# Optimization experiments

Measured on AMD Instinct MI355X. Metric: run time of the kernel, lower is better.

The kernel has to match this reference:

```python
import jax, jax.numpy as jnp
import numpy as np

N = 65536      # tokens
D = 512        # input_dim
H = 8          # num_heads
HD = 64        # head_dim
FF = 2048      # hidden_dim
EPS = 1e-5


def _layer_norm(x, g, b):
    mu = jnp.mean(x, axis=-1, keepdims=True)
    var = jnp.mean(jnp.square(x - mu), axis=-1, keepdims=True)
    return (x - mu) * jax.lax.rsqrt(var + EPS) * g + b


def setup_inputs() -> dict:
    key = jax.random.key(0)
    ks = jax.random.split(key, 12)
    s_d = 1.0 / np.sqrt(D)
    s_f = 1.0 / np.sqrt(FF)
    return {
        "x":   jax.random.normal(ks[0], (N, D), jnp.float32),
        # Linear weights stored [in, out] (transpose of torch's [out, in])
        "Wq":  jax.random.uniform(ks[1], (D, D), jnp.float32, -s_d, s_d),
        "bq":  jnp.zeros((D,), jnp.float32),
        "Wk":  jax.random.uniform(ks[2], (D, D), jnp.float32, -s_d, s_d),
        "bk":  jnp.zeros((D,), jnp.float32),
        "Wv":  jax.random.uniform(ks[3], (D, D), jnp.float32, -s_d, s_d),
        "bv":  jnp.zeros((D,), jnp.float32),
        "ln1_g": jnp.ones((D,), jnp.float32),
        "ln1_b": jnp.zeros((D,), jnp.float32),
        "W1":  jax.random.uniform(ks[4], (D, FF), jnp.float32, -s_d, s_d),
        "b1":  jnp.zeros((FF,), jnp.float32),
        "W2":  jax.random.uniform(ks[5], (FF, D), jnp.float32, -s_f, s_f),
        "b2":  jnp.zeros((D,), jnp.float32),
        "ln2_g": jnp.ones((D,), jnp.float32),
        "ln2_b": jnp.zeros((D,), jnp.float32),
    }


def reference(x, Wq, bq, Wk, bk, Wv, bv, ln1_g, ln1_b, W1, b1, W2, b2, ln2_g, ln2_b):
    n = x.shape[0]
    # --- multi-head attention (per-token head mixing, as in source) ---
    q = (x @ Wq + bq).reshape(n, H, HD)
    k = (x @ Wk + bk).reshape(n, H, HD)
    v = (x @ Wv + bv).reshape(n, H, HD)
    # score[n] = q[n] @ k[n]^T : [H, H] per token
    score = jnp.einsum("nhd,ngd->nhg", q, k) / jnp.sqrt(jnp.float32(HD))
    attn = jax.nn.softmax(score, axis=-1)
    ctx = jnp.einsum("nhg,ngd->nhd", attn, v).reshape(n, D)
    y = _layer_norm(x + ctx, ln1_g, ln1_b)
    # --- feed forward with residual + layer norm ---
    h = jax.nn.relu(y @ W1 + b1)
    z = h @ W2 + b2 + y
    return _layer_norm(z, ln2_g, ln2_b)
```

## Files before the change

kernel.cpp:

```cpp
#include <hip/hip_runtime.h>
#include <cstdint>


typedef __attribute__((ext_vector_type(8))) short bf16x8;
typedef __attribute__((ext_vector_type(4))) float f32x4;
typedef __attribute__((ext_vector_type(8))) unsigned short u16x8;

__device__ __forceinline__ float bf2f(unsigned short u) {
  union { unsigned int i; float f; } v; v.i = ((unsigned int)u) << 16; return v.f;
}
__device__ __forceinline__ unsigned short f2bf(float f) {
  union { float f; unsigned int i; } v; v.f = f;
  unsigned int r = v.i + 0x7FFFu + ((v.i >> 16) & 1u);
  return (unsigned short)(r >> 16);
}

#define GLD16(g, l)                                                         \
  __builtin_amdgcn_global_load_lds(                                         \
      (const __attribute__((address_space(1))) void*)(g),                   \
      (__attribute__((address_space(3))) void*)(l), 16, 0, 0)

__global__ __launch_bounds__(256) void cast_f32_bf16(
    const float* __restrict__ in, ushort* __restrict__ out) {
  const size_t i = (size_t)blockIdx.x * 256 + threadIdx.x;
  const float4* p = (const float4*)in + i * 2;
  float4 a = p[0], b = p[1];
  u16x8 r;
  r[0] = f2bf(a.x); r[1] = f2bf(a.y); r[2] = f2bf(a.z); r[3] = f2bf(a.w);
  r[4] = f2bf(b.x); r[5] = f2bf(b.y); r[6] = f2bf(b.z); r[7] = f2bf(b.w);
  ((u16x8*)out)[i] = r;
}

__global__ __launch_bounds__(256) void transpose_cast(
    const float* __restrict__ W, ushort* __restrict__ Wt,
    int K, int Nn, int rowoff, int ldt) {
  __shared__ float tile[32][33];
  const int tx = threadIdx.x & 31, ty = threadIdx.x >> 5;
  const int nb = blockIdx.x * 32, kb = blockIdx.y * 32;
#pragma unroll
  for (int s = 0; s < 4; ++s)
    tile[ty + 8 * s][tx] = W[(size_t)(kb + ty + 8 * s) * Nn + nb + tx];
  __syncthreads();
#pragma unroll
  for (int s = 0; s < 4; ++s)
    Wt[(size_t)(rowoff + nb + ty + 8 * s) * ldt + kb + tx] =
        f2bf(tile[tx][ty + 8 * s]);
}

template <int EPI>
__global__ __launch_bounds__(512, 2) void gemm_bt(
    const ushort* __restrict__ A, const ushort* __restrict__ Bt,
    int N, int K, void* __restrict__ Cout,
    const float* __restrict__ bias0, const float* __restrict__ bias1,
    const float* __restrict__ bias2, const ushort* __restrict__ resid) {
  constexpr int BK = 32;
  __shared__ __align__(16) ushort lds[4 * 16384];
  const int tid = threadIdx.x;
  const int wid = tid >> 6, lane = tid & 63;
  const int wm = wid >> 2, wn = wid & 3;

  const int gx = gridDim.x;
  const int nwg = gx * gridDim.y;
  const int orig = blockIdx.y * gx + blockIdx.x;
  const int q = nwg >> 3, r = nwg & 7;
  const int xcd = orig & 7, loc = orig >> 3;
  const int swz = (xcd < r) ? (xcd * (q + 1) + loc)
                            : (r * (q + 1) + (xcd - r) * q + loc);
  const size_t m0 = (size_t)(swz / gx) * 256;
  const size_t n0 = (size_t)(swz % gx) * 256;
  const int NT = K / BK;

  const int sgcol = (((tid & 3) - ((tid >> 3) & 3)) & 3) << 3;
  const ushort* a0 = A + (m0 + (tid >> 2)) * (size_t)K + sgcol;
  const ushort* b0 = Bt + (n0 + (tid >> 2)) * (size_t)K + sgcol;
  const size_t rowK = 128 * (size_t)K;
  ushort* ldst = &lds[tid * 8];

#define STAGE_A(t)                                                          \
  {                                                                         \
    ushort* d = ldst + ((t) & 3) * 16384;                                   \
    const ushort* g = a0 + (size_t)(t) * BK;                                \
    GLD16(g, d);                                                            \
    GLD16(g + rowK, d + 4096);                                              \
  }
#define STAGE_B(t)                                                          \
  {                                                                         \
    ushort* d = ldst + ((t) & 3) * 16384 + 8192;                            \
    const ushort* g = b0 + (size_t)(t) * BK;                                \
    GLD16(g, d);                                                            \
    GLD16(g + rowK, d + 4096);                                              \
  }

  const int cswz = ((((lane >> 4) + ((lane >> 1) & 3)) & 3) << 3);
  const int arow = wm * 128 + (lane & 15);
  const int brow = wn * 64 + (lane & 15);

  f32x4 acc[8][4] = {};

  STAGE_A(0); STAGE_B(0);
  STAGE_A(1); STAGE_B(1);
  STAGE_A(2); STAGE_B(2);

  for (int t = 0; t < NT; ++t) {
    if (t < NT - 2) {
      asm volatile("s_waitcnt vmcnt(8)" ::: "memory");
    } else if (t == NT - 2) {
      asm volatile("s_waitcnt vmcnt(4)" ::: "memory");
    } else {
      asm volatile("s_waitcnt vmcnt(0)" ::: "memory");
    }
    __builtin_amdgcn_s_barrier();

    const ushort* lA = &lds[(t & 3) * 16384];
    const ushort* lB = lA + 8192;

    bf16x8 af[4], bfr[4];
#pragma unroll
    for (int mi = 0; mi < 4; ++mi)
      af[mi] = *(const bf16x8*)&lA[(arow + mi * 16) * 32 + cswz];
#pragma unroll
    for (int ni = 0; ni < 4; ++ni)
      bfr[ni] = *(const bf16x8*)&lB[(brow + ni * 16) * 32 + cswz];
    if (t + 3 < NT) STAGE_A(t + 3);
    __builtin_amdgcn_s_setprio(1);
#pragma unroll
    for (int mi = 0; mi < 4; ++mi)
#pragma unroll
      for (int ni = 0; ni < 4; ++ni)
        acc[mi][ni] = __builtin_amdgcn_mfma_f32_16x16x32_bf16(
            af[mi], bfr[ni], acc[mi][ni], 0, 0, 0);
    __builtin_amdgcn_s_setprio(0);
    __builtin_amdgcn_s_barrier();

    bf16x8 ag[4];
#pragma unroll
    for (int mi = 0; mi < 4; ++mi)
      ag[mi] = *(const bf16x8*)&lA[(arow + (mi + 4) * 16) * 32 + cswz];
    if (t + 3 < NT) STAGE_B(t + 3);
    __builtin_amdgcn_s_setprio(1);
#pragma unroll
    for (int mi = 0; mi < 4; ++mi)
#pragma unroll
      for (int ni = 0; ni < 4; ++ni)
        acc[mi + 4][ni] = __builtin_amdgcn_mfma_f32_16x16x32_bf16(
            ag[mi], bfr[ni], acc[mi + 4][ni], 0, 0, 0);
    __builtin_amdgcn_s_setprio(0);
  }
#undef STAGE_A
#undef STAGE_B

  const int lm = lane & 15, lq = lane >> 4;
  size_t col[4];
  float bv[4];
#pragma unroll
  for (int ni = 0; ni < 4; ++ni) {
    col[ni] = n0 + wn * 64 + ni * 16 + lm;
    if (EPI == 0) {
      const float* bp = (n0 < 512) ? bias0 : ((n0 < 1024) ? bias1 : bias2);
      bv[ni] = bp[col[ni] & 511];
    } else {
      bv[ni] = bias0[col[ni]];
    }
  }
#pragma unroll
  for (int mi = 0; mi < 8; ++mi) {
#pragma unroll
    for (int j = 0; j < 4; ++j) {
      const size_t row = m0 + wm * 128 + mi * 16 + lq * 4 + j;
#pragma unroll
      for (int ni = 0; ni < 4; ++ni) {
        float v = acc[mi][ni][j] + bv[ni];
        if (EPI == 0) {
          ((ushort*)Cout)[row * N + col[ni]] = f2bf(v);
        } else if (EPI == 1) {
          ((ushort*)Cout)[row * N + col[ni]] = f2bf(fmaxf(v, 0.f));
        } else {
          v += bf2f(resid[row * N + col[ni]]);
          ((float*)Cout)[row * N + col[ni]] = v;
        }
      }
    }
  }
}

__global__ __launch_bounds__(256) void attn_ln1(
    const ushort* __restrict__ qkv, const float* __restrict__ x,
    const float* __restrict__ g1, const float* __restrict__ b1,
    ushort* __restrict__ y) {
  const int lane = threadIdx.x & 63;
  const size_t t = (size_t)blockIdx.x * 4 + (threadIdx.x >> 6);
  const ushort* base = qkv + t * 1536;
  float qd[8], kd[8], vd[8];
#pragma unroll
  for (int h = 0; h < 8; ++h) {
    qd[h] = bf2f(base[h * 64 + lane]);
    kd[h] = bf2f(base[512 + h * 64 + lane]);
    vd[h] = bf2f(base[1024 + h * 64 + lane]);
  }

  const bool lb0 = lane & 1, lb1 = lane & 2, lb2 = lane & 4;
  const bool lb3 = lane & 8, lb4 = lane & 16, lb5 = lane & 32;

  float c1[32];
#pragma unroll
  for (int f = 0; f < 32; ++f) {
    const int i0 = 2 * f, i1 = 2 * f + 1;
    const float a0 = qd[i0 >> 3] * kd[i0 & 7];
    const float a1 = qd[i1 >> 3] * kd[i1 & 7];
    const float keep = lb0 ? a1 : a0;
    const float send = lb0 ? a0 : a1;
    c1[f] = keep + __shfl_xor(send, 1, 64);
  }
  float c2[16];
#pragma unroll
  for (int f = 0; f < 16; ++f) {
    const float keep = lb1 ? c1[2 * f + 1] : c1[2 * f];
    const float send = lb1 ? c1[2 * f] : c1[2 * f + 1];
    c2[f] = keep + __shfl_xor(send, 2, 64);
  }
  float c3[8];
#pragma unroll
  for (int f = 0; f < 8; ++f) {
    const float keep = lb2 ? c2[2 * f + 1] : c2[2 * f];
    const float send = lb2 ? c2[2 * f] : c2[2 * f + 1];
    c3[f] = keep + __shfl_xor(send, 4, 64);
  }
  float c4[4];
#pragma unroll
  for (int f = 0; f < 4; ++f) {
    const float keep = lb3 ? c3[2 * f + 1] : c3[2 * f];
    const float send = lb3 ? c3[2 * f] : c3[2 * f + 1];
    c4[f] = keep + __shfl_xor(send, 8, 64);
  }
  float c5[2];
#pragma unroll
  for (int f = 0; f < 2; ++f) {
    const float keep = lb4 ? c4[2 * f + 1] : c4[2 * f];
    const float send = lb4 ? c4[2 * f] : c4[2 * f + 1];
    c5[f] = keep + __shfl_xor(send, 16, 64);
  }
  const float keep = lb5 ? c5[1] : c5[0];
  const float send = lb5 ? c5[0] : c5[1];
  const float s = keep + __shfl_xor(send, 32, 64);

  float mx = s;
  mx = fmaxf(mx, __shfl_xor(mx, 1, 64));
  mx = fmaxf(mx, __shfl_xor(mx, 2, 64));
  mx = fmaxf(mx, __shfl_xor(mx, 4, 64));
  const float e = __expf((s - mx) * 0.125f);
  float sum = e;
  sum += __shfl_xor(sum, 1, 64);
  sum += __shfl_xor(sum, 2, 64);
  sum += __shfl_xor(sum, 4, 64);
  const float a = e * __builtin_amdgcn_rcpf(sum);

  const int ai = __float_as_int(a);
  float r[8];
#pragma unroll
  for (int h = 0; h < 8; ++h) {
    float c = 0.f;
#pragma unroll
    for (int g = 0; g < 8; ++g) {
      const float w = __int_as_float(__builtin_amdgcn_readlane(ai, h * 8 + g));
      c = fmaf(w, vd[g], c);
    }
    r[h] = x[t * 512 + h * 64 + lane] + c;
  }

  float sm = 0.f, sq = 0.f;
#pragma unroll
  for (int h = 0; h < 8; ++h) { sm += r[h]; sq += r[h] * r[h]; }
#pragma unroll
  for (int m = 1; m < 64; m <<= 1) {
    sm += __shfl_xor(sm, m, 64);
    sq += __shfl_xor(sq, m, 64);
  }
  const float mu = sm * (1.f / 512.f);
  const float var = sq * (1.f / 512.f) - mu * mu;
  const float rs = rsqrtf(var + 1e-5f);
#pragma unroll
  for (int h = 0; h < 8; ++h) {
    const int d = h * 64 + lane;
    y[t * 512 + d] = f2bf((r[h] - mu) * rs * g1[d] + b1[d]);
  }
}

__global__ __launch_bounds__(256) void ln_out(
    const float* __restrict__ z, const float* __restrict__ g2,
    const float* __restrict__ b2, float* __restrict__ out) {
  const int lane = threadIdx.x & 63;
  const size_t t = (size_t)blockIdx.x * 4 + (threadIdx.x >> 6);
  const float4* zp = (const float4*)(z + t * 512);
  const float4 r0 = zp[lane], r1 = zp[lane + 64];
  float sm = r0.x + r0.y + r0.z + r0.w + r1.x + r1.y + r1.z + r1.w;
  float sq = r0.x * r0.x + r0.y * r0.y + r0.z * r0.z + r0.w * r0.w +
             r1.x * r1.x + r1.y * r1.y + r1.z * r1.z + r1.w * r1.w;
#pragma unroll
  for (int m = 1; m < 64; m <<= 1) {
    sm += __shfl_xor(sm, m, 64);
    sq += __shfl_xor(sq, m, 64);
  }
  const float mu = sm * (1.f / 512.f);
  const float rs = rsqrtf(sq * (1.f / 512.f) - mu * mu + 1e-5f);
  const float4* g4 = (const float4*)g2;
  const float4* b4 = (const float4*)b2;
  float4* o4 = (float4*)(out + t * 512);
  const float4 ga = g4[lane], gb = g4[lane + 64];
  const float4 ba = b4[lane], bb = b4[lane + 64];
  float4 oa, ob;
  oa.x = (r0.x - mu) * rs * ga.x + ba.x;
  oa.y = (r0.y - mu) * rs * ga.y + ba.y;
  oa.z = (r0.z - mu) * rs * ga.z + ba.z;
  oa.w = (r0.w - mu) * rs * ga.w + ba.w;
  ob.x = (r1.x - mu) * rs * gb.x + bb.x;
  ob.y = (r1.y - mu) * rs * gb.y + bb.y;
  ob.z = (r1.z - mu) * rs * gb.z + bb.z;
  ob.w = (r1.w - mu) * rs * gb.w + bb.w;
  o4[lane] = oa;
  o4[lane + 64] = ob;
}

extern "C" void kernel_launch(void* const* d_in, const int* in_sizes, int n_in,
                              void* d_out, int out_size, void* d_ws,
                              size_t ws_size, hipStream_t stream) {
  const float* x    = (const float*)d_in[0];
  const float* Wq   = (const float*)d_in[1];
  const float* bq   = (const float*)d_in[2];
  const float* Wk   = (const float*)d_in[3];
  const float* bk   = (const float*)d_in[4];
  const float* Wv   = (const float*)d_in[5];
  const float* bv   = (const float*)d_in[6];
  const float* ln1g = (const float*)d_in[7];
  const float* ln1b = (const float*)d_in[8];
  const float* W1   = (const float*)d_in[9];
  const float* b1   = (const float*)d_in[10];
  const float* W2   = (const float*)d_in[11];
  const float* b2   = (const float*)d_in[12];
  const float* ln2g = (const float*)d_in[13];
  const float* ln2b = (const float*)d_in[14];
  float* out = (float*)d_out;

  const int Ntok = in_sizes[0] / 512;

  char* ws = (char*)d_ws;
  ushort* Wqkvt = (ushort*)ws;
  ushort* W1t   = Wqkvt + (size_t)1536 * 512;
  ushort* W2t   = W1t + (size_t)2048 * 512;
  const size_t woff = ((size_t)1536 * 512 + (size_t)2048 * 512 +
                       (size_t)512 * 2048) * 2;

  size_t avail = (ws_size > woff) ? (ws_size - woff) : 0;
  long long Cll = (long long)(avail / 9216);
  Cll = (Cll / 256) * 256;
  if (Cll > 32768) Cll = 32768;
  if (Cll > Ntok) Cll = Ntok;
  if (Cll < 256) Cll = 256;
  const int C = (int)Cll;

  char* cb = ws + woff;
  ushort* xb  = (ushort*)cb;
  ushort* y   = xb + (size_t)C * 512;
  ushort* qkv = y + (size_t)C * 512;
  ushort* hb  = qkv + (size_t)C * 1536;
  float*  z   = (float*)qkv;

  transpose_cast<<<dim3(16, 16), dim3(256), 0, stream>>>(Wq, Wqkvt, 512, 512, 0, 512);
  transpose_cast<<<dim3(16, 16), dim3(256), 0, stream>>>(Wk, Wqkvt, 512, 512, 512, 512);
  transpose_cast<<<dim3(16, 16), dim3(256), 0, stream>>>(Wv, Wqkvt, 512, 512, 1024, 512);
  transpose_cast<<<dim3(64, 16), dim3(256), 0, stream>>>(W1, W1t, 512, 2048, 0, 512);
  transpose_cast<<<dim3(16, 64), dim3(256), 0, stream>>>(W2, W2t, 2048, 512, 0, 2048);

  for (int t0 = 0; t0 < Ntok; t0 += C) {
    const int Cc = (Ntok - t0 < C) ? (Ntok - t0) : C;
    const float* xc = x + (size_t)t0 * 512;

    cast_f32_bf16<<<dim3((Cc * 512) / 2048), dim3(256), 0, stream>>>(xc, xb);

    gemm_bt<0><<<dim3(1536 / 256, Cc / 256), dim3(512), 0, stream>>>(
        xb, Wqkvt, 1536, 512, qkv, bq, bk, bv, nullptr);

    attn_ln1<<<dim3(Cc / 4), dim3(256), 0, stream>>>(qkv, xc, ln1g, ln1b, y);

    gemm_bt<1><<<dim3(2048 / 256, Cc / 256), dim3(512), 0, stream>>>(
        y, W1t, 2048, 512, hb, b1, nullptr, nullptr, nullptr);

    gemm_bt<2><<<dim3(512 / 256, Cc / 256), dim3(512), 0, stream>>>(
        hb, W2t, 512, 2048, z, b2, nullptr, nullptr, y);

    ln_out<<<dim3(Cc / 4), dim3(256), 0, stream>>>(
        z, ln2g, ln2b, out + (size_t)t0 * 512);
  }
}
```

Baseline: 666.8 us.

## Make GEMM persistent with cross-tile prefetch pipeline over 256 workgroups

Converts the tiled GEMM into a persistent kernel launched with 256 workgroups, each looping over output tiles strided by 256 and treating all k-steps of all its tiles as one continuous pipeline. Loads for the next tile are issued during the previous tile's tail, so the prologue/epilogue bubbles and per-block launch cost are removed, and the epilogue runs inline before the accumulators are zeroed. It drops the XCD-aware tile swizzle, hardcodes ntLog for only K=512 or 2048, and stores the epilogue while the next prefetches are in flight, which may hurt L2 locality and register pressure.

```diff
diff --git a/kernel.cpp b/kernel.cpp
--- a/kernel.cpp
+++ b/kernel.cpp
@@ -50,7 +50,7 @@
 template <int EPI>
 __global__ __launch_bounds__(512, 2) void gemm_bt(
     const ushort* __restrict__ A, const ushort* __restrict__ Bt,
-    int N, int K, void* __restrict__ Cout,
+    int M, int N, int K, void* __restrict__ Cout,
     const float* __restrict__ bias0, const float* __restrict__ bias1,
     const float* __restrict__ bias2, const ushort* __restrict__ resid) {
   constexpr int BK = 32;
@@ -59,34 +59,42 @@
   const int wid = tid >> 6, lane = tid & 63;
   const int wm = wid >> 2, wn = wid & 3;
 
-  const int gx = gridDim.x;
-  const int nwg = gx * gridDim.y;
-  const int orig = blockIdx.y * gx + blockIdx.x;
-  const int q = nwg >> 3, r = nwg & 7;
-  const int xcd = orig & 7, loc = orig >> 3;
-  const int swz = (xcd < r) ? (xcd * (q + 1) + loc)
-                            : (r * (q + 1) + (xcd - r) * q + loc);
-  const size_t m0 = (size_t)(swz / gx) * 256;
-  const size_t n0 = (size_t)(swz % gx) * 256;
+  const int NX = N >> 8;
+  const int tiles = (M >> 8) * NX;
+  const int b = blockIdx.x;
+  const int nOut = (tiles - b + 255) >> 8;
+  if (nOut <= 0) return;
   const int NT = K / BK;
+  const int ntLog = (NT == 16) ? 4 : 6;
+  const int Ttot = nOut * NT;
 
   const int sgcol = (((tid & 3) - ((tid >> 3) & 3)) & 3) << 3;
-  const ushort* a0 = A + (m0 + (tid >> 2)) * (size_t)K + sgcol;
-  const ushort* b0 = Bt + (n0 + (tid >> 2)) * (size_t)K + sgcol;
+  const int thrRow = tid >> 2;
   const size_t rowK = 128 * (size_t)K;
   ushort* ldst = &lds[tid * 8];
 
-#define STAGE_A(t)                                                          \
+#define TILE_COORDS(tau, sm0, sn0, sk0)                                     \
+  const int ot_ = (tau) >> ntLog;                                           \
+  const int T_ = b + (ot_ << 8);                                            \
+  const size_t sm0 = (size_t)(T_ / NX) << 8;                                \
+  const size_t sn0 = (size_t)(T_ % NX) << 8;                                \
+  const size_t sk0 = (size_t)((tau) & (NT - 1)) * BK;
+
+#define STAGE_A(tau)                                                        \
   {                                                                         \
-    ushort* d = ldst + ((t) & 3) * 16384;                                   \
-    const ushort* g = a0 + (size_t)(t) * BK;                                \
+    TILE_COORDS(tau, sm0, sn0, sk0)                                         \
+    (void)sn0;                                                              \
+    const ushort* g = A + (sm0 + thrRow) * (size_t)K + sgcol + sk0;         \
+    ushort* d = ldst + ((tau) & 3) * 16384;                                 \
     GLD16(g, d);                                                            \
     GLD16(g + rowK, d + 4096);                                              \
   }
-#define STAGE_B(t)                                                          \
+#define STAGE_B(tau)                                                        \
   {                                                                         \
-    ushort* d = ldst + ((t) & 3) * 16384 + 8192;                            \
-    const ushort* g = b0 + (size_t)(t) * BK;                                \
+    TILE_COORDS(tau, sm0, sn0, sk0)                                         \
+    (void)sm0;                                                              \
+    const ushort* g = Bt + (sn0 + thrRow) * (size_t)K + sgcol + sk0;        \
+    ushort* d = ldst + ((tau) & 3) * 16384 + 8192;                          \
     GLD16(g, d);                                                            \
     GLD16(g + rowK, d + 4096);                                              \
   }
@@ -94,6 +102,7 @@
   const int cswz = ((((lane >> 4) + ((lane >> 1) & 3)) & 3) << 3);
   const int arow = wm * 128 + (lane & 15);
   const int brow = wn * 64 + (lane & 15);
+  const int lm = lane & 15, lq = lane >> 4;
 
   f32x4 acc[8][4] = {};
 
@@ -101,17 +110,17 @@
   STAGE_A(1); STAGE_B(1);
   STAGE_A(2); STAGE_B(2);
 
-  for (int t = 0; t < NT; ++t) {
-    if (t < NT - 2) {
+  for (int tau = 0; tau < Ttot; ++tau) {
+    if (tau < Ttot - 2) {
       asm volatile("s_waitcnt vmcnt(8)" ::: "memory");
-    } else if (t == NT - 2) {
+    } else if (tau == Ttot - 2) {
       asm volatile("s_waitcnt vmcnt(4)" ::: "memory");
     } else {
       asm volatile("s_waitcnt vmcnt(0)" ::: "memory");
     }
     __builtin_amdgcn_s_barrier();
 
-    const ushort* lA = &lds[(t & 3) * 16384];
+    const ushort* lA = &lds[(tau & 3) * 16384];
     const ushort* lB = lA + 8192;
 
     bf16x8 af[4], bfr[4];
@@ -121,7 +130,7 @@
 #pragma unroll
     for (int ni = 0; ni < 4; ++ni)
       bfr[ni] = *(const bf16x8*)&lB[(brow + ni * 16) * 32 + cswz];
-    if (t + 3 < NT) STAGE_A(t + 3);
+    if (tau + 3 < Ttot) STAGE_A(tau + 3);
     __builtin_amdgcn_s_setprio(1);
 #pragma unroll
     for (int mi = 0; mi < 4; ++mi)
@@ -136,7 +145,7 @@
 #pragma unroll
     for (int mi = 0; mi < 4; ++mi)
       ag[mi] = *(const bf16x8*)&lA[(arow + (mi + 4) * 16) * 32 + cswz];
-    if (t + 3 < NT) STAGE_B(t + 3);
+    if (tau + 3 < Ttot) STAGE_B(tau + 3);
     __builtin_amdgcn_s_setprio(1);
 #pragma unroll
     for (int mi = 0; mi < 4; ++mi)
@@ -145,42 +154,52 @@
         acc[mi + 4][ni] = __builtin_amdgcn_mfma_f32_16x16x32_bf16(
             ag[mi], bfr[ni], acc[mi + 4][ni], 0, 0, 0);
     __builtin_amdgcn_s_setprio(0);
+
+    if ((tau & (NT - 1)) == NT - 1) {
+      TILE_COORDS(tau, m0, n0, k0)
+      (void)k0;
+      size_t col[4];
+      float bv[4];
+#pragma unroll
+      for (int ni = 0; ni < 4; ++ni) {
+        col[ni] = n0 + wn * 64 + ni * 16 + lm;
+        if (EPI == 0) {
+          const float* bp = (n0 < 512) ? bias0 : ((n0 < 1024) ? bias1 : bias2);
+          bv[ni] = bp[col[ni] & 511];
+        } else {
+          bv[ni] = bias0[col[ni]];
+        }
+      }
+#pragma unroll
+      for (int mi = 0; mi < 8; ++mi) {
+#pragma unroll
+        for (int j = 0; j < 4; ++j) {
+          const size_t row = m0 + wm * 128 + mi * 16 + lq * 4 + j;
+#pragma unroll
+          for (int ni = 0; ni < 4; ++ni) {
+            float v = acc[mi][ni][j] + bv[ni];
+            if (EPI == 0) {
+              ((ushort*)Cout)[row * N + col[ni]] = f2bf(v);
+            } else if (EPI == 1) {
+              ((ushort*)Cout)[row * N + col[ni]] = f2bf(fmaxf(v, 0.f));
+            } else {
+              v += bf2f(resid[row * N + col[ni]]);
+              ((float*)Cout)[row * N + col[ni]] = v;
+            }
+          }
+        }
+      }
+#pragma unroll
+      for (int mi = 0; mi < 8; ++mi)
+#pragma unroll
+        for (int ni = 0; ni < 4; ++ni)
+#pragma unroll
+          for (int j = 0; j < 4; ++j) acc[mi][ni][j] = 0.f;
+    }
   }
 #undef STAGE_A
 #undef STAGE_B
-
-  const int lm = lane & 15, lq = lane >> 4;
-  size_t col[4];
-  float bv[4];
-#pragma unroll
-  for (int ni = 0; ni < 4; ++ni) {
-    col[ni] = n0 + wn * 64 + ni * 16 + lm;
-    if (EPI == 0) {
-      const float* bp = (n0 < 512) ? bias0 : ((n0 < 1024) ? bias1 : bias2);
-      bv[ni] = bp[col[ni] & 511];
-    } else {
-      bv[ni] = bias0[col[ni]];
-    }
-  }
-#pragma unroll
-  for (int mi = 0; mi < 8; ++mi) {
-#pragma unroll
-    for (int j = 0; j < 4; ++j) {
-      const size_t row = m0 + wm * 128 + mi * 16 + lq * 4 + j;
-#pragma unroll
-      for (int ni = 0; ni < 4; ++ni) {
-        float v = acc[mi][ni][j] + bv[ni];
-        if (EPI == 0) {
-          ((ushort*)Cout)[row * N + col[ni]] = f2bf(v);
-        } else if (EPI == 1) {
-          ((ushort*)Cout)[row * N + col[ni]] = f2bf(fmaxf(v, 0.f));
-        } else {
-          v += bf2f(resid[row * N + col[ni]]);
-          ((float*)Cout)[row * N + col[ni]] = v;
-        }
-      }
-    }
-  }
+#undef TILE_COORDS
 }
 
 __global__ __launch_bounds__(256) void attn_ln1(
@@ -376,16 +395,16 @@
 
     cast_f32_bf16<<<dim3((Cc * 512) / 2048), dim3(256), 0, stream>>>(xc, xb);
 
-    gemm_bt<0><<<dim3(1536 / 256, Cc / 256), dim3(512), 0, stream>>>(
-        xb, Wqkvt, 1536, 512, qkv, bq, bk, bv, nullptr);
+    gemm_bt<0><<<dim3(256), dim3(512), 0, stream>>>(
+        xb, Wqkvt, Cc, 1536, 512, qkv, bq, bk, bv, nullptr);
 
     attn_ln1<<<dim3(Cc / 4), dim3(256), 0, stream>>>(qkv, xc, ln1g, ln1b, y);
 
-    gemm_bt<1><<<dim3(2048 / 256, Cc / 256), dim3(512), 0, stream>>>(
-        y, W1t, 2048, 512, hb, b1, nullptr, nullptr, nullptr);
-
-    gemm_bt<2><<<dim3(512 / 256, Cc / 256), dim3(512), 0, stream>>>(
-        hb, W2t, 512, 2048, z, b2, nullptr, nullptr, y);
+    gemm_bt<1><<<dim3(256), dim3(512), 0, stream>>>(
+        y, W1t, Cc, 2048, 512, hb, b1, nullptr, nullptr, nullptr);
+
+    gemm_bt<2><<<dim3(256), dim3(512), 0, stream>>>(
+        hb, W2t, Cc, 512, 2048, z, b2, nullptr, nullptr, y);
 
     ln_out<<<dim3(Cc / 4), dim3(256), 0, stream>>>(
         z, ln2g, ln2b, out + (size_t)t0 * 512);
```

Result: slower. 690.3 us (+3.5%).

## Split GEMM k-step into four barrier phases and store FFN output as bf16

Applied to the files above, without the earlier changes.

The GEMM main loop now runs as four phases per k-step. Each phase loads two A fragments, issues one quarter of the next tile's global-to-LDS loads, and runs eight MFMAs between barriers, so loads are spread more evenly against compute. The second FFN GEMM now writes its residual-added output as bf16 instead of fp32, and ln_out reads bf16, which halves that intermediate traffic. attn_ln1 now reads the bf16 copy of x for the residual instead of fp32, trading precision for less bandwidth. The extra barriers per k-step add synchronisation cost.

```diff
diff --git a/kernel.cpp b/kernel.cpp
--- a/kernel.cpp
+++ b/kernel.cpp
@@ -62,10 +62,10 @@
   const int gx = gridDim.x;
   const int nwg = gx * gridDim.y;
   const int orig = blockIdx.y * gx + blockIdx.x;
-  const int q = nwg >> 3, r = nwg & 7;
+  const int q8 = nwg >> 3, r8 = nwg & 7;
   const int xcd = orig & 7, loc = orig >> 3;
-  const int swz = (xcd < r) ? (xcd * (q + 1) + loc)
-                            : (r * (q + 1) + (xcd - r) * q + loc);
+  const int swz = (xcd < r8) ? (xcd * (q8 + 1) + loc)
+                             : (r8 * (q8 + 1) + (xcd - r8) * q8 + loc);
   const size_t m0 = (size_t)(swz / gx) * 256;
   const size_t n0 = (size_t)(swz % gx) * 256;
   const int NT = K / BK;
@@ -76,19 +76,12 @@
   const size_t rowK = 128 * (size_t)K;
   ushort* ldst = &lds[tid * 8];
 
-#define STAGE_A(t)                                                          \
+#define STAGE_SLOT(t, sl)                                                   \
   {                                                                         \
-    ushort* d = ldst + ((t) & 3) * 16384;                                   \
-    const ushort* g = a0 + (size_t)(t) * BK;                                \
+    ushort* d = ldst + ((t) & 3) * 16384 + (sl) * 4096;                     \
+    const ushort* g = (((sl) < 2) ? a0 : b0) + (size_t)(t) * BK +           \
+                      (((sl) & 1) ? rowK : 0);                              \
     GLD16(g, d);                                                            \
-    GLD16(g + rowK, d + 4096);                                              \
-  }
-#define STAGE_B(t)                                                          \
-  {                                                                         \
-    ushort* d = ldst + ((t) & 3) * 16384 + 8192;                            \
-    const ushort* g = b0 + (size_t)(t) * BK;                                \
-    GLD16(g, d);                                                            \
-    GLD16(g + rowK, d + 4096);                                              \
   }
 
   const int cswz = ((((lane >> 4) + ((lane >> 1) & 3)) & 3) << 3);
@@ -97,9 +90,30 @@
 
   f32x4 acc[8][4] = {};
 
-  STAGE_A(0); STAGE_B(0);
-  STAGE_A(1); STAGE_B(1);
-  STAGE_A(2); STAGE_B(2);
+#pragma unroll
+  for (int pt = 0; pt < 3; ++pt) {
+    STAGE_SLOT(pt, 0); STAGE_SLOT(pt, 1);
+    STAGE_SLOT(pt, 2); STAGE_SLOT(pt, 3);
+  }
+
+#define PHASE(pi)                                                           \
+  {                                                                         \
+    bf16x8 y0 = *(const bf16x8*)&lA[(arow + (2 * (pi)) * 16) * 32 + cswz];  \
+    bf16x8 y1 = *(const bf16x8*)&lA[(arow + (2 * (pi) + 1) * 16) * 32 + cswz]; \
+    if (pf) STAGE_SLOT(t3, pi);                                             \
+    __builtin_amdgcn_s_barrier();                                           \
+    __builtin_amdgcn_s_setprio(1);                                          \
+    _Pragma("unroll")                                                       \
+    for (int ni = 0; ni < 4; ++ni)                                          \
+      acc[2 * (pi)][ni] = __builtin_amdgcn_mfma_f32_16x16x32_bf16(          \
+          y0, bfr[ni], acc[2 * (pi)][ni], 0, 0, 0);                         \
+    _Pragma("unroll")                                                       \
+    for (int ni = 0; ni < 4; ++ni)                                          \
+      acc[2 * (pi) + 1][ni] = __builtin_amdgcn_mfma_f32_16x16x32_bf16(      \
+          y1, bfr[ni], acc[2 * (pi) + 1][ni], 0, 0, 0);                     \
+    __builtin_amdgcn_s_setprio(0);                                          \
+    __builtin_amdgcn_s_barrier();                                           \
+  }
 
   for (int t = 0; t < NT; ++t) {
     if (t < NT - 2) {
@@ -113,41 +127,21 @@
 
     const ushort* lA = &lds[(t & 3) * 16384];
     const ushort* lB = lA + 8192;
-
-    bf16x8 af[4], bfr[4];
-#pragma unroll
-    for (int mi = 0; mi < 4; ++mi)
-      af[mi] = *(const bf16x8*)&lA[(arow + mi * 16) * 32 + cswz];
+    const bool pf = (t + 3 < NT);
+    const int t3 = t + 3;
+
+    bf16x8 bfr[4];
 #pragma unroll
     for (int ni = 0; ni < 4; ++ni)
       bfr[ni] = *(const bf16x8*)&lB[(brow + ni * 16) * 32 + cswz];
-    if (t + 3 < NT) STAGE_A(t + 3);
-    __builtin_amdgcn_s_setprio(1);
-#pragma unroll
-    for (int mi = 0; mi < 4; ++mi)
-#pragma unroll
-      for (int ni = 0; ni < 4; ++ni)
-        acc[mi][ni] = __builtin_amdgcn_mfma_f32_16x16x32_bf16(
-            af[mi], bfr[ni], acc[mi][ni], 0, 0, 0);
-    __builtin_amdgcn_s_setprio(0);
-    __builtin_amdgcn_s_barrier();
-
-    bf16x8 ag[4];
-#pragma unroll
-    for (int mi = 0; mi < 4; ++mi)
-      ag[mi] = *(const bf16x8*)&lA[(arow + (mi + 4) * 16) * 32 + cswz];
-    if (t + 3 < NT) STAGE_B(t + 3);
-    __builtin_amdgcn_s_setprio(1);
-#pragma unroll
-    for (int mi = 0; mi < 4; ++mi)
-#pragma unroll
-      for (int ni = 0; ni < 4; ++ni)
-        acc[mi + 4][ni] = __builtin_amdgcn_mfma_f32_16x16x32_bf16(
-            ag[mi], bfr[ni], acc[mi + 4][ni], 0, 0, 0);
-    __builtin_amdgcn_s_setprio(0);
-  }
-#undef STAGE_A
-#undef STAGE_B
+
+    PHASE(0)
+    PHASE(1)
+    PHASE(2)
+    PHASE(3)
+  }
+#undef PHASE
+#undef STAGE_SLOT
 
   const int lm = lane & 15, lq = lane >> 4;
   size_t col[4];
@@ -176,7 +170,7 @@
           ((ushort*)Cout)[row * N + col[ni]] = f2bf(fmaxf(v, 0.f));
         } else {
           v += bf2f(resid[row * N + col[ni]]);
-          ((float*)Cout)[row * N + col[ni]] = v;
+          ((ushort*)Cout)[row * N + col[ni]] = f2bf(v);
         }
       }
     }
@@ -184,7 +178,7 @@
 }
 
 __global__ __launch_bounds__(256) void attn_ln1(
-    const ushort* __restrict__ qkv, const float* __restrict__ x,
+    const ushort* __restrict__ qkv, const ushort* __restrict__ xb,
     const float* __restrict__ g1, const float* __restrict__ b1,
     ushort* __restrict__ y) {
   const int lane = threadIdx.x & 63;
@@ -264,7 +258,7 @@
       const float w = __int_as_float(__builtin_amdgcn_readlane(ai, h * 8 + g));
       c = fmaf(w, vd[g], c);
     }
-    r[h] = x[t * 512 + h * 64 + lane] + c;
+    r[h] = bf2f(xb[t * 512 + h * 64 + lane]) + c;
   }
 
   float sm = 0.f, sq = 0.f;
@@ -286,15 +280,19 @@
 }
 
 __global__ __launch_bounds__(256) void ln_out(
-    const float* __restrict__ z, const float* __restrict__ g2,
+    const ushort* __restrict__ zb, const float* __restrict__ g2,
     const float* __restrict__ b2, float* __restrict__ out) {
   const int lane = threadIdx.x & 63;
   const size_t t = (size_t)blockIdx.x * 4 + (threadIdx.x >> 6);
-  const float4* zp = (const float4*)(z + t * 512);
-  const float4 r0 = zp[lane], r1 = zp[lane + 64];
-  float sm = r0.x + r0.y + r0.z + r0.w + r1.x + r1.y + r1.z + r1.w;
-  float sq = r0.x * r0.x + r0.y * r0.y + r0.z * r0.z + r0.w * r0.w +
-             r1.x * r1.x + r1.y * r1.y + r1.z * r1.z + r1.w * r1.w;
+  const u16x8 v = ((const u16x8*)(zb + t * 512))[lane];
+  float r[8];
+  float sm = 0.f, sq = 0.f;
+#pragma unroll
+  for (int j = 0; j < 8; ++j) {
+    r[j] = bf2f(v[j]);
+    sm += r[j];
+    sq += r[j] * r[j];
+  }
 #pragma unroll
   for (int m = 1; m < 64; m <<= 1) {
     sm += __shfl_xor(sm, m, 64);
@@ -302,22 +300,23 @@
   }
   const float mu = sm * (1.f / 512.f);
   const float rs = rsqrtf(sq * (1.f / 512.f) - mu * mu + 1e-5f);
-  const float4* g4 = (const float4*)g2;
-  const float4* b4 = (const float4*)b2;
-  float4* o4 = (float4*)(out + t * 512);
-  const float4 ga = g4[lane], gb = g4[lane + 64];
-  const float4 ba = b4[lane], bb = b4[lane + 64];
+  const int d0 = lane * 8;
+  const float4 ga = *(const float4*)(g2 + d0);
+  const float4 gb = *(const float4*)(g2 + d0 + 4);
+  const float4 ba = *(const float4*)(b2 + d0);
+  const float4 bb = *(const float4*)(b2 + d0 + 4);
   float4 oa, ob;
-  oa.x = (r0.x - mu) * rs * ga.x + ba.x;
-  oa.y = (r0.y - mu) * rs * ga.y + ba.y;
-  oa.z = (r0.z - mu) * rs * ga.z + ba.z;
-  oa.w = (r0.w - mu) * rs * ga.w + ba.w;
-  ob.x = (r1.x - mu) * rs * gb.x + bb.x;
-  ob.y = (r1.y - mu) * rs * gb.y + bb.y;
-  ob.z = (r1.z - mu) * rs * gb.z + bb.z;
-  ob.w = (r1.w - mu) * rs * gb.w + bb.w;
-  o4[lane] = oa;
-  o4[lane + 64] = ob;
+  oa.x = (r[0] - mu) * rs * ga.x + ba.x;
+  oa.y = (r[1] - mu) * rs * ga.y + ba.y;
+  oa.z = (r[2] - mu) * rs * ga.z + ba.z;
+  oa.w = (r[3] - mu) * rs * ga.w + ba.w;
+  ob.x = (r[4] - mu) * rs * gb.x + bb.x;
+  ob.y = (r[5] - mu) * rs * gb.y + bb.y;
+  ob.z = (r[6] - mu) * rs * gb.z + bb.z;
+  ob.w = (r[7] - mu) * rs * gb.w + bb.w;
+  float* o = out + t * 512 + d0;
+  *(float4*)o = oa;
+  *(float4*)(o + 4) = ob;
 }
 
 extern "C" void kernel_launch(void* const* d_in, const int* in_sizes, int n_in,
@@ -362,7 +361,7 @@
   ushort* y   = xb + (size_t)C * 512;
   ushort* qkv = y + (size_t)C * 512;
   ushort* hb  = qkv + (size_t)C * 1536;
-  float*  z   = (float*)qkv;
+  ushort* zb  = qkv;
 
   transpose_cast<<<dim3(16, 16), dim3(256), 0, stream>>>(Wq, Wqkvt, 512, 512, 0, 512);
   transpose_cast<<<dim3(16, 16), dim3(256), 0, stream>>>(Wk, Wqkvt, 512, 512, 512, 512);
@@ -379,15 +378,15 @@
     gemm_bt<0><<<dim3(1536 / 256, Cc / 256), dim3(512), 0, stream>>>(
         xb, Wqkvt, 1536, 512, qkv, bq, bk, bv, nullptr);
 
-    attn_ln1<<<dim3(Cc / 4), dim3(256), 0, stream>>>(qkv, xc, ln1g, ln1b, y);
+    attn_ln1<<<dim3(Cc / 4), dim3(256), 0, stream>>>(qkv, xb, ln1g, ln1b, y);
 
     gemm_bt<1><<<dim3(2048 / 256, Cc / 256), dim3(512), 0, stream>>>(
         y, W1t, 2048, 512, hb, b1, nullptr, nullptr, nullptr);
 
     gemm_bt<2><<<dim3(512 / 256, Cc / 256), dim3(512), 0, stream>>>(
-        hb, W2t, 512, 2048, z, b2, nullptr, nullptr, y);
+        hb, W2t, 512, 2048, zb, b2, nullptr, nullptr, y);
 
     ln_out<<<dim3(Cc / 4), dim3(256), 0, stream>>>(
-        z, ln2g, ln2b, out + (size_t)t0 * 512);
-  }
-}
+        zb, ln2g, ln2b, out + (size_t)t0 * 512);
+  }
+}
```

New measurement: 638.9 us. 4.2% less time.
